# Optimization experiments

Measured on AMD Instinct MI355X. Metric: run time of the kernel, lower is better.

The kernel has to match this reference:

```python
import jax, jax.numpy as jnp
import numpy as np
from jax import lax

V, E, HD, T = 32000, 256, 256, 4   # vocab, embed dim, lstm hidden (bidir total), tagset (BMES)
H = HD // 2                        # hidden per direction
B, S = 64, 1024


def setup_inputs() -> dict:
    key = jax.random.key(0)
    ks = jax.random.split(key, 16)
    sc = 0.1
    return {
        "sentences": jax.random.randint(ks[0], (B, S), 0, V, dtype=jnp.int32),
        "embed": jax.random.normal(ks[1], (V, E), jnp.float32) * sc,
        "w_ih_f": jax.random.normal(ks[2], (4 * H, E), jnp.float32) * sc,
        "w_hh_f": jax.random.normal(ks[3], (4 * H, H), jnp.float32) * sc,
        "b_ih_f": jax.random.normal(ks[4], (4 * H,), jnp.float32) * sc,
        "b_hh_f": jax.random.normal(ks[5], (4 * H,), jnp.float32) * sc,
        "w_ih_r": jax.random.normal(ks[6], (4 * H, E), jnp.float32) * sc,
        "w_hh_r": jax.random.normal(ks[7], (4 * H, H), jnp.float32) * sc,
        "b_ih_r": jax.random.normal(ks[8], (4 * H,), jnp.float32) * sc,
        "b_hh_r": jax.random.normal(ks[9], (4 * H,), jnp.float32) * sc,
        "w_out": jax.random.normal(ks[10], (T, HD), jnp.float32) * sc,
        "b_out": jax.random.normal(ks[11], (T,), jnp.float32) * sc,
        "start_t": jax.random.normal(ks[12], (T,), jnp.float32) * sc,
        "end_t": jax.random.normal(ks[13], (T,), jnp.float32) * sc,
        "trans": jax.random.normal(ks[14], (T, T), jnp.float32) * sc,
    }


def _lstm_pass(x, w_ih, w_hh, b_ih, b_hh):
    # x: [S, B, E]; PyTorch gate order i, f, g, o; zero initial state.
    bsz = x.shape[1]
    hdim = w_hh.shape[1]
    b = b_ih + b_hh

    def step(carry, xt):
        h, c = carry
        z = xt @ w_ih.T + h @ w_hh.T + b  # [B, 4H]
        i, f, g, o = jnp.split(z, 4, axis=-1)
        c = jax.nn.sigmoid(f) * c + jax.nn.sigmoid(i) * jnp.tanh(g)
        h = jax.nn.sigmoid(o) * jnp.tanh(c)
        return (h, c), h

    init = (jnp.zeros((bsz, hdim), x.dtype), jnp.zeros((bsz, hdim), x.dtype))
    _, hs = lax.scan(step, init, x)
    return hs  # [S, B, H]


def _emissions(sentences, embed, w_ih_f, w_hh_f, b_ih_f, b_hh_f,
               w_ih_r, w_hh_r, b_ih_r, b_hh_r, w_out, b_out):
    x = embed[sentences]                # [B, S, E]
    xs = jnp.transpose(x, (1, 0, 2))    # [S, B, E]
    hf = _lstm_pass(xs, w_ih_f, w_hh_f, b_ih_f, b_hh_f)
    hr = _lstm_pass(xs[::-1], w_ih_r, w_hh_r, b_ih_r, b_hh_r)[::-1]
    h = jnp.concatenate([hf, hr], axis=-1)        # [S, B, 2H]
    return h @ w_out.T + b_out                    # [S, B, T] emissions


def _viterbi_decode(feats, start_t, end_t, trans):
    # feats: [S, B, T] (no mask: all sequences full length, matching crf.decode on dense batch)
    score0 = start_t + feats[0]  # [B, T]

    def fwd_step(score, emit):
        nxt = score[:, :, None] + trans[None, :, :] + emit[:, None, :]  # [B, Tprev, Tcur]
        return jnp.max(nxt, axis=1), jnp.argmax(nxt, axis=1)

    final, bps = lax.scan(fwd_step, score0, feats[1:])  # bps: [S-1, B, T]
    final = final + end_t
    last = jnp.argmax(final, axis=1)  # [B]

    def back_step(tag, bp):
        prev = jnp.take_along_axis(bp, tag[:, None], axis=1)[:, 0]
        return prev, prev

    _, path_head = lax.scan(back_step, last, bps, reverse=True)  # [S-1, B], tags at t=0..S-2
    path = jnp.concatenate([path_head, last[None]], axis=0)      # [S, B]
    return jnp.transpose(path, (1, 0)).astype(jnp.int32)         # [B, S]


def reference(sentences, embed, w_ih_f, w_hh_f, b_ih_f, b_hh_f,
              w_ih_r, w_hh_r, b_ih_r, b_hh_r, w_out, b_out,
              start_t, end_t, trans):
    feats = _emissions(sentences, embed, w_ih_f, w_hh_f, b_ih_f, b_hh_f,
                       w_ih_r, w_hh_r, b_ih_r, b_hh_r, w_out, b_out)
    return _viterbi_decode(feats, start_t, end_t, trans)
```

## Files before the change

### kernel.cpp

```cpp
#include <hip/hip_runtime.h>
#include <cstdint>
#include <cstddef>

#define SLEN 1024
#define BATCH 64
#define EDIM 256
#define HDIM 128
#define GDIM 512
#define NTAG 4

typedef float f2 __attribute__((ext_vector_type(2)));
typedef float f4 __attribute__((ext_vector_type(4)));


__device__ __forceinline__ float sigm_f(float x) {
    return 1.0f / (1.0f + __expf(-x));
}
__device__ __forceinline__ float tanh_f(float x) {
    return 1.0f - 2.0f / (1.0f + __expf(2.0f * x));
}

template <int CTRL>
__device__ __forceinline__ float quad_perm(float x) {
    return __int_as_float(
        __builtin_amdgcn_mov_dpp(__float_as_int(x), CTRL, 0xF, 0xF, true));
}
#define QP_XOR1 0xB1
#define QP_XOR2 0x4E
#define QP_MIR8 0x141
#define QP_BC0  0x00
#define QP_BC1  0x55
#define QP_BC2  0xAA
#define QP_BC3  0xFF

__device__ __forceinline__ void gemm_body(
    float* smem, int mt, int cp,
    const int* __restrict__ sent, const float* __restrict__ embed,
    const float* __restrict__ w_ih_f, const float* __restrict__ w_ih_r,
    const float* __restrict__ b_ih_f, const float* __restrict__ b_hh_f,
    const float* __restrict__ b_ih_r, const float* __restrict__ b_hh_r,
    float* __restrict__ Z, int base_f, int base_r)
{
    float* As = smem;
    const int t  = threadIdx.x;
    const int tm = t >> 8;
    const int tt = t & 255;
    float* Bs = smem + 4096 + tm * 4096;

    const int nt  = cp * 2 + tm;
    const int dir = nt >> 2;
    const float* W  = dir ? w_ih_r : w_ih_f;
    const float* bi = dir ? b_ih_r : b_ih_f;
    const float* bh = dir ? b_hh_r : b_hh_f;
    const int ncol = (nt & 3) * 128;
    const int r0   = mt * 128;

    const int sra = t & 127;
    const int qa  = t >> 7;
    const int r_loc = r0 + sra;
    const int s_loc = r_loc >> 6;
    const int b_    = r_loc & 63;
    const int s_glob = (dir ? base_r : base_f) + s_loc;
    const int tok = sent[b_ * SLEN + s_glob];
    const float* arow = embed + (size_t)tok * EDIM + qa * 8;

    const int srb = tt & 127;
    const int hb  = tt >> 7;
    const float* brow = W + (size_t)(ncol + srb) * EDIM + hb * 16;

    const int tx = tt & 15, ty = tt >> 4;

    f2 acc[8][4];
    #pragma unroll
    for (int i = 0; i < 8; ++i)
        #pragma unroll
        for (int jj = 0; jj < 4; ++jj) acc[i][jj] = (f2)(0.0f);

    for (int kt = 0; kt < 8; ++kt) {
        const int k0 = kt * 32;
        __syncthreads();
        {
            float4 v0 = *(const float4*)(arow + k0);
            float4 v1 = *(const float4*)(arow + k0 + 4);
            const int kk = qa * 8;
            As[(kk + 0) * 128 + sra] = v0.x;
            As[(kk + 1) * 128 + sra] = v0.y;
            As[(kk + 2) * 128 + sra] = v0.z;
            As[(kk + 3) * 128 + sra] = v0.w;
            As[(kk + 4) * 128 + sra] = v1.x;
            As[(kk + 5) * 128 + sra] = v1.y;
            As[(kk + 6) * 128 + sra] = v1.z;
            As[(kk + 7) * 128 + sra] = v1.w;
        }
        #pragma unroll
        for (int i = 0; i < 4; ++i) {
            float4 v = *(const float4*)(brow + k0 + i * 4);
            const int kk = hb * 16 + i * 4;
            Bs[(kk + 0) * 128 + srb] = v.x;
            Bs[(kk + 1) * 128 + srb] = v.y;
            Bs[(kk + 2) * 128 + srb] = v.z;
            Bs[(kk + 3) * 128 + srb] = v.w;
        }
        __syncthreads();

        #pragma unroll 8
        for (int k = 0; k < 32; ++k) {
            const f4 a0  = *(const f4*)&As[k * 128 + ty * 4];
            const f4 a1  = *(const f4*)&As[k * 128 + 64 + ty * 4];
            const f4 bq0 = *(const f4*)&Bs[k * 128 + tx * 4];
            const f4 bq1 = *(const f4*)&Bs[k * 128 + 64 + tx * 4];
            float av[8] = {a0.x, a0.y, a0.z, a0.w, a1.x, a1.y, a1.z, a1.w};
            f2 bv[4];
            bv[0] = __builtin_shufflevector(bq0, bq0, 0, 1);
            bv[1] = __builtin_shufflevector(bq0, bq0, 2, 3);
            bv[2] = __builtin_shufflevector(bq1, bq1, 0, 1);
            bv[3] = __builtin_shufflevector(bq1, bq1, 2, 3);
            #pragma unroll
            for (int i = 0; i < 8; ++i) {
                f2 as; as.x = av[i]; as.y = av[i];
                #pragma unroll
                for (int jj = 0; jj < 4; ++jj)
                    acc[i][jj] += as * bv[jj];
            }
        }
    }

    float bias0[4], bias1[4];
    #pragma unroll
    for (int j = 0; j < 4; ++j) {
        bias0[j] = bi[ncol + tx * 4 + j] + bh[ncol + tx * 4 + j];
        bias1[j] = bi[ncol + 64 + tx * 4 + j] + bh[ncol + 64 + tx * 4 + j];
    }

    #pragma unroll
    for (int i = 0; i < 8; ++i) {
        const int row = r0 + ((i < 4) ? (ty * 4 + i) : (64 + ty * 4 + i - 4));
        float* zp = Z + (size_t)row * 1024 + dir * 512 + ncol;
        float4 o0, o1;
        o0.x = acc[i][0].x + bias0[0]; o0.y = acc[i][0].y + bias0[1];
        o0.z = acc[i][1].x + bias0[2]; o0.w = acc[i][1].y + bias0[3];
        o1.x = acc[i][2].x + bias1[0]; o1.y = acc[i][2].y + bias1[1];
        o1.z = acc[i][3].x + bias1[2]; o1.w = acc[i][3].y + bias1[3];
        *(float4*)(zp + tx * 4)      = o0;
        *(float4*)(zp + 64 + tx * 4) = o1;
    }
}

__device__ __forceinline__ void lstm_body(
    float* smem,
    const float* __restrict__ Z, const float* __restrict__ w_hh_f,
    const float* __restrict__ w_hh_r, float* __restrict__ H,
    float* __restrict__ ST, int base_f, int base_r, int L, int first)
{
    float* sh_h = smem;

    const int bid = blockIdx.x;
    const int b   = bid & 63;
    const int dir = bid >> 6;
    const int q   = threadIdx.x;
    const int p   = q & 7;
    const int Q   = q >> 3;
    const int gt  = p & 3;
    const int hi  = p >> 2;
    const int u   = Q + hi * 64;

    const float* Whh = dir ? w_hh_r : w_hh_f;

    f2 w2[8][8];
    #pragma unroll
    for (int pr = 0; pr < 8; ++pr) {
        const int uu = (pr & 4) ? (Q + 64) : Q;
        const int gg = pr & 3;
        const f2* src =
            (const f2*)(Whh + ((size_t)(gg * 128 + uu) * 128 + p * 16));
        #pragma unroll
        for (int i = 0; i < 8; ++i) w2[pr][i] = src[i];
    }
    #pragma unroll
    for (int pr = 0; pr < 8; ++pr)
        #pragma unroll
        for (int i = 0; i < 8; ++i)
            asm volatile("" : "+v"(w2[pr][i]));

    float* stp = ST + (size_t)(dir * 64 + b) * 256;
    if (q < 128)
        sh_h[(q >> 5) * 36 + (q & 31)] = first ? 0.0f : stp[q];
    float c = first ? 0.0f : stp[128 + u];

    const ptrdiff_t zstride = dir ? -65536 : 65536;
    const float* zp0 = Z + (size_t)b * 1024 + dir * 512
                     + (dir ? (size_t)(L - 1) * 65536 : 0) + gt * 128 + u;
    const ptrdiff_t hstride = dir ? -16384 : 16384;
    float* hg = H + ((size_t)(dir ? (base_r + L - 1) : base_f) * 64 + b) * 256
              + dir * 128 + u;

    const bool k4 = (p & 4) != 0;
    const bool k2 = (p & 2) != 0;
    const bool k1 = (p & 1) != 0;
    const float gsc  = (gt == 2) ? 2.0f : 1.0f;
    const float gofs = (gt == 2) ? -1.0f : 0.0f;
    const int shr = (p >> 1) * 36 + (p & 1) * 16;
    const int shw = (u >> 5) * 36 + (u & 31);

    float zcur[4], znxt[4];
    {
        const float* zp = zp0;
        #pragma unroll
        for (int dt = 0; dt < 4; ++dt) { zcur[dt] = *zp; zp += zstride; }
    }
    __syncthreads();

    float hlast = 0.0f;

    for (int t0 = 0; t0 < L; t0 += 4) {
        const bool more = (t0 + 4 < L);
        if (more) {
            const float* zp = zp0 + (ptrdiff_t)(t0 + 4) * zstride;
            #pragma unroll
            for (int dt = 0; dt < 4; ++dt) { znxt[dt] = *zp; zp += zstride; }
        }

        #pragma unroll
        for (int dt = 0; dt < 4; ++dt) {
            const f4* hp = (const f4*)(sh_h + (dt & 1) * 160 + shr);
            f2 hv[8];
            #pragma unroll
            for (int i = 0; i < 4; ++i) {
                f4 v = hp[i];
                hv[2 * i]     = __builtin_shufflevector(v, v, 0, 1);
                hv[2 * i + 1] = __builtin_shufflevector(v, v, 2, 3);
            }
            float s[8];
            #pragma unroll
            for (int pr = 0; pr < 8; ++pr) {
                f2 a = (f2)(0.0f);
                #pragma unroll
                for (int i = 0; i < 8; ++i) a += w2[pr][i] * hv[i];
                s[pr] = a.x + a.y;
            }
            float K1[4];
            #pragma unroll
            for (int j = 0; j < 4; ++j) {
                float keep = k4 ? s[j + 4] : s[j];
                float send = k4 ? s[j] : s[j + 4];
                K1[j] = keep + quad_perm<QP_MIR8>(send);
            }
            float K2[2];
            #pragma unroll
            for (int j = 0; j < 2; ++j) {
                float keep = k2 ? K1[j + 2] : K1[j];
                float send = k2 ? K1[j] : K1[j + 2];
                K2[j] = keep + quad_perm<QP_XOR2>(send);
            }
            float keep3 = k1 ? K2[1] : K2[0];
            float send3 = k1 ? K2[0] : K2[1];
            float zv = keep3 + quad_perm<QP_XOR1>(send3) + zcur[dt];

            float sgv = sigm_f(zv * gsc);
            float act = fmaf(sgv, gsc, gofs);

            float a_i = quad_perm<QP_BC0>(act);
            float a_f = quad_perm<QP_BC1>(act);
            float a_g = quad_perm<QP_BC2>(act);
            float a_o = quad_perm<QP_BC3>(act);
            c = a_f * c + a_i * a_g;
            float h = a_o * tanh_f(c);
            hlast = h;

            if (gt == 0) {
                sh_h[((dt + 1) & 1) * 160 + shw] = h;
                *hg = h;
            }
            hg += hstride;
            __syncthreads();
        }

        if (more) {
            #pragma unroll
            for (int dt = 0; dt < 4; ++dt) zcur[dt] = znxt[dt];
        }
    }

    if (gt == 0) {
        stp[u] = hlast;
        stp[128 + u] = c;
    }
}

__global__ __launch_bounds__(512) void fused_lstm_gemm(
    const int* __restrict__ sent, const float* __restrict__ embed,
    const float* __restrict__ w_ih_f, const float* __restrict__ w_ih_r,
    const float* __restrict__ b_ih_f, const float* __restrict__ b_hh_f,
    const float* __restrict__ b_ih_r, const float* __restrict__ b_hh_r,
    float* __restrict__ Zw, int gbase_f, int gbase_r, int mtiles,
    const float* __restrict__ Zr, const float* __restrict__ w_hh_f,
    const float* __restrict__ w_hh_r, float* __restrict__ H,
    float* __restrict__ ST, int lbase_f, int lbase_r, int L, int first)
{
    __shared__ __align__(16) float smem[12288];

    if (blockIdx.x < 128) {
        lstm_body(smem, Zr, w_hh_f, w_hh_r, H, ST, lbase_f, lbase_r, L, first);
    } else {
        const int g  = blockIdx.x - 128;
        const int mt = g % mtiles;
        const int cp = g / mtiles;
        gemm_body(smem, mt, cp, sent, embed, w_ih_f, w_ih_r,
                  b_ih_f, b_hh_f, b_ih_r, b_hh_r, Zw, gbase_f, gbase_r);
    }
}

__global__ __launch_bounds__(512) void gemm_zin(
    const int* __restrict__ sent, const float* __restrict__ embed,
    const float* __restrict__ w_ih_f, const float* __restrict__ w_ih_r,
    const float* __restrict__ b_ih_f, const float* __restrict__ b_hh_f,
    const float* __restrict__ b_ih_r, const float* __restrict__ b_hh_r,
    float* __restrict__ Z, int base_f, int base_r)
{
    __shared__ __align__(16) float smem[12288];
    gemm_body(smem, blockIdx.x, blockIdx.y, sent, embed, w_ih_f, w_ih_r,
              b_ih_f, b_hh_f, b_ih_r, b_hh_r, Z, base_f, base_r);
}

__global__ __launch_bounds__(256) void emissions_k(
    const float* __restrict__ H, const float* __restrict__ w_out,
    const float* __restrict__ b_out, float* __restrict__ F)
{
    const int gid = blockIdx.x * 256 + threadIdx.x;
    const int r   = gid >> 2;
    const int tg  = gid & 3;
    const float4* h4 = (const float4*)(H + (size_t)r * 256);
    const float4* w4 = (const float4*)(w_out + (size_t)tg * 256);
    float a0 = 0.f, a1 = 0.f, a2 = 0.f, a3 = 0.f;
    #pragma unroll 8
    for (int k = 0; k < 64; ++k) {
        float4 h = h4[k], w = w4[k];
        a0 = fmaf(h.x, w.x, a0); a1 = fmaf(h.y, w.y, a1);
        a2 = fmaf(h.z, w.z, a2); a3 = fmaf(h.w, w.w, a3);
    }
    F[gid] = ((a0 + a1) + (a2 + a3)) + b_out[tg];
}

__device__ __forceinline__ unsigned compose_map(unsigned a, unsigned b) {
    unsigned r = 0;
    #pragma unroll
    for (int jj = 0; jj < 4; ++jj) {
        unsigned bj = (b >> (jj * 8)) & 3u;
        unsigned aj = (a >> (bj * 8)) & 3u;
        r |= aj << (jj * 8);
    }
    return r;
}

__global__ __launch_bounds__(64) void viterbi_k(
    const float* __restrict__ F, const float* __restrict__ start_t,
    const float* __restrict__ end_t, const float* __restrict__ trans,
    int* __restrict__ out)
{
    const int b    = blockIdx.x;
    const int lane = threadIdx.x;
    __shared__ __align__(16) float sfeat[SLEN][NTAG];
    __shared__ unsigned sbp[SLEN];

    #pragma unroll
    for (int i = 0; i < 16; ++i) {
        int s = i * 64 + lane;
        ((float4*)sfeat)[s] = *(const float4*)(F + ((size_t)s * BATCH + b) * NTAG);
    }
    __syncthreads();

    const int cur = lane & 3;
    float tr0 = trans[0 * 4 + cur], tr1 = trans[1 * 4 + cur];
    float tr2 = trans[2 * 4 + cur], tr3 = trans[3 * 4 + cur];
    float sc = start_t[cur] + sfeat[0][cur];

    for (int s = 1; s < SLEN; ++s) {
        float ft = sfeat[s][cur];
        float s0 = __shfl(sc, 0), s1 = __shfl(sc, 1);
        float s2 = __shfl(sc, 2), s3 = __shfl(sc, 3);
        float c0 = s0 + tr0, c1 = s1 + tr1, c2 = s2 + tr2, c3 = s3 + tr3;
        float best = c0; int arg = 0;
        if (c1 > best) { best = c1; arg = 1; }
        if (c2 > best) { best = c2; arg = 2; }
        if (c3 > best) { best = c3; arg = 3; }
        sc = best + ft;
        unsigned bp = (unsigned)arg;
        unsigned b0 = __shfl(bp, 0), b1 = __shfl(bp, 1);
        unsigned b2 = __shfl(bp, 2), b3 = __shfl(bp, 3);
        if (lane == 0) sbp[s] = b0 | (b1 << 8) | (b2 << 16) | (b3 << 24);
    }
    sc += end_t[cur];
    float f0 = __shfl(sc, 0), f1 = __shfl(sc, 1);
    float f2v = __shfl(sc, 2), f3 = __shfl(sc, 3);
    int last = 0; float bb = f0;
    if (f1 > bb)  { bb = f1;  last = 1; }
    if (f2v > bb) { bb = f2v; last = 2; }
    if (f3 > bb)  { bb = f3;  last = 3; }
    __syncthreads();

    unsigned m[16];
    #pragma unroll
    for (int k = 0; k < 16; ++k) {
        int s = lane * 16 + k;
        m[k] = (s >= 1) ? sbp[s] : 0x03020100u;
    }
    unsigned G = m[15];
    #pragma unroll
    for (int k = 14; k >= 0; --k) G = compose_map(m[k], G);
    unsigned R = G;
    #pragma unroll
    for (int d = 1; d < 64; d <<= 1) {
        unsigned oo = __shfl_down(R, d);
        if (lane + d < 64) R = compose_map(R, oo);
    }
    unsigned P = __shfl_down(R, 1);
    if (lane == 63) P = 0x03020100u;

    int tcur = (int)((P >> (last * 8)) & 3u);
    int* ob = out + b * SLEN + lane * 16;
    ob[15] = tcur;
    #pragma unroll
    for (int k = 15; k >= 1; --k) {
        tcur = (int)((m[k] >> (tcur * 8)) & 3u);
        ob[k - 1] = tcur;
    }
}

extern "C" void kernel_launch(void* const* d_in, const int* in_sizes, int n_in,
                              void* d_out, int out_size, void* d_ws, size_t ws_size,
                              hipStream_t stream)
{
    const int*   sent    = (const int*)d_in[0];
    const float* embed   = (const float*)d_in[1];
    const float* w_ih_f  = (const float*)d_in[2];
    const float* w_hh_f  = (const float*)d_in[3];
    const float* b_ih_f  = (const float*)d_in[4];
    const float* b_hh_f  = (const float*)d_in[5];
    const float* w_ih_r  = (const float*)d_in[6];
    const float* w_hh_r  = (const float*)d_in[7];
    const float* b_ih_r  = (const float*)d_in[8];
    const float* b_hh_r  = (const float*)d_in[9];
    const float* w_out   = (const float*)d_in[10];
    const float* b_out   = (const float*)d_in[11];
    const float* start_t = (const float*)d_in[12];
    const float* end_t   = (const float*)d_in[13];
    const float* trans   = (const float*)d_in[14];
    int* out = (int*)d_out;

    const size_t H_FLOATS  = (size_t)SLEN * BATCH * 256;
    const size_t F_FLOATS  = (size_t)SLEN * BATCH * NTAG;
    const size_t ST_FLOATS = (size_t)2 * BATCH * 256;
    const size_t FIXED = H_FLOATS + F_FLOATS + ST_FLOATS;

    int L = 0;
    for (int cand = 256; cand >= 32; cand >>= 1) {
        size_t need = ((size_t)2 * cand * BATCH * 1024 + FIXED) * sizeof(float);
        if (need <= ws_size) { L = cand; break; }
    }

    if (L > 0) {
        const int nch = SLEN / L;
        const int mtiles = (L * BATCH) / 128;
        float* Z0 = (float*)d_ws;
        float* Z1 = Z0 + (size_t)L * BATCH * 1024;
        float* H  = Z1 + (size_t)L * BATCH * 1024;
        float* F  = H + H_FLOATS;
        float* ST = F + F_FLOATS;
        float* Zb[2] = {Z0, Z1};

        gemm_zin<<<dim3(mtiles, 4), 512, 0, stream>>>(
            sent, embed, w_ih_f, w_ih_r, b_ih_f, b_hh_f, b_ih_r, b_hh_r,
            Zb[0], 0, SLEN - L);

        for (int c = 0; c < nch; ++c) {
            const int lbase_f = c * L;
            const int lbase_r = SLEN - (c + 1) * L;
            const int hasg = (c + 1 < nch);
            const int gbase_f = (c + 1) * L;
            const int gbase_r = SLEN - (c + 2) * L;
            const int grid = hasg ? (128 + mtiles * 4) : 128;
            fused_lstm_gemm<<<grid, 512, 0, stream>>>(
                sent, embed, w_ih_f, w_ih_r, b_ih_f, b_hh_f, b_ih_r, b_hh_r,
                Zb[(c + 1) & 1], hasg ? gbase_f : 0, hasg ? gbase_r : 0, mtiles,
                Zb[c & 1], w_hh_f, w_hh_r, H, ST, lbase_f, lbase_r, L,
                c == 0 ? 1 : 0);
        }

        emissions_k<<<1024, 256, 0, stream>>>(H, w_out, b_out, F);
        viterbi_k<<<64, 64, 0, stream>>>(F, start_t, end_t, trans, out);
    } else {
        int Ls = SLEN;
        while (Ls > 32) {
            size_t need = ((size_t)Ls * BATCH * 1024 + FIXED) * sizeof(float);
            if (need <= ws_size) break;
            Ls >>= 1;
        }
        const int nch = SLEN / Ls;
        const int mtiles = (Ls * BATCH) / 128;
        float* Z  = (float*)d_ws;
        float* H  = Z + (size_t)Ls * BATCH * 1024;
        float* F  = H + H_FLOATS;
        float* ST = F + F_FLOATS;

        for (int c = 0; c < nch; ++c) {
            const int base_f = c * Ls;
            const int base_r = SLEN - (c + 1) * Ls;
            gemm_zin<<<dim3(mtiles, 4), 512, 0, stream>>>(
                sent, embed, w_ih_f, w_ih_r, b_ih_f, b_hh_f, b_ih_r, b_hh_r,
                Z, base_f, base_r);
            fused_lstm_gemm<<<128, 512, 0, stream>>>(
                sent, embed, w_ih_f, w_ih_r, b_ih_f, b_hh_f, b_ih_r, b_hh_r,
                Z, 0, 0, mtiles,
                Z, w_hh_f, w_hh_r, H, ST, base_f, base_r, Ls, c == 0 ? 1 : 0);
        }
        emissions_k<<<1024, 256, 0, stream>>>(H, w_out, b_out, F);
        viterbi_k<<<64, 64, 0, stream>>>(F, start_t, end_t, trans, out);
    }
}
```

Measured before the change: 1.190 ms.

## Precompute per-vocab input-gate table and run the LSTM as one persistent kernel

Adds a path that computes embed·W_ihᵀ plus biases once per vocabulary entry into a 32000×1024 table. A single LSTM kernel then walks the whole sequence and gathers gate pre-activations by token id, prefetching four steps ahead. This replaces the per-chunk input GEMM over all B·S tokens and the chunked LSTM launches with their state save and restore. The GEMM shrinks from 65536 rows to 32000, at the cost of a large workspace table and scattered row reads during the recurrence. The old chunked path remains as a fallback when the workspace is too small.

```diff
diff --git a/kernel.cpp b/kernel.cpp
--- a/kernel.cpp
+++ b/kernel.cpp
@@ -8,6 +8,7 @@
 #define HDIM 128
 #define GDIM 512
 #define NTAG 4
+#define VOCAB 32000
 
 typedef float f2 __attribute__((ext_vector_type(2)));
 typedef float f4 __attribute__((ext_vector_type(4)));
@@ -33,20 +34,22 @@
 #define QP_BC2  0xAA
 #define QP_BC3  0xFF
 
-__device__ __forceinline__ void gemm_body(
-    float* smem, int mt, int cp,
-    const int* __restrict__ sent, const float* __restrict__ embed,
+__global__ __launch_bounds__(512) void table_k(
+    const float* __restrict__ embed,
     const float* __restrict__ w_ih_f, const float* __restrict__ w_ih_r,
     const float* __restrict__ b_ih_f, const float* __restrict__ b_hh_f,
     const float* __restrict__ b_ih_r, const float* __restrict__ b_hh_r,
-    float* __restrict__ Z, int base_f, int base_r)
-{
+    float* __restrict__ T)
+{
+    __shared__ __align__(16) float smem[12288];
     float* As = smem;
     const int t  = threadIdx.x;
     const int tm = t >> 8;
     const int tt = t & 255;
     float* Bs = smem + 4096 + tm * 4096;
 
+    const int mt  = blockIdx.x;
+    const int cp  = blockIdx.y;
     const int nt  = cp * 2 + tm;
     const int dir = nt >> 2;
     const float* W  = dir ? w_ih_r : w_ih_f;
@@ -57,12 +60,7 @@
 
     const int sra = t & 127;
     const int qa  = t >> 7;
-    const int r_loc = r0 + sra;
-    const int s_loc = r_loc >> 6;
-    const int b_    = r_loc & 63;
-    const int s_glob = (dir ? base_r : base_f) + s_loc;
-    const int tok = sent[b_ * SLEN + s_glob];
-    const float* arow = embed + (size_t)tok * EDIM + qa * 8;
+    const float* arow = embed + (size_t)(r0 + sra) * EDIM + qa * 8;
 
     const int srb = tt & 127;
     const int hb  = tt >> 7;
@@ -135,7 +133,7 @@
     #pragma unroll
     for (int i = 0; i < 8; ++i) {
         const int row = r0 + ((i < 4) ? (ty * 4 + i) : (64 + ty * 4 + i - 4));
-        float* zp = Z + (size_t)row * 1024 + dir * 512 + ncol;
+        float* zp = T + (size_t)row * 1024 + dir * 512 + ncol;
         float4 o0, o1;
         o0.x = acc[i][0].x + bias0[0]; o0.y = acc[i][0].y + bias0[1];
         o0.z = acc[i][1].x + bias0[2]; o0.w = acc[i][1].y + bias0[3];
@@ -146,13 +144,14 @@
     }
 }
 
-__device__ __forceinline__ void lstm_body(
-    float* smem,
-    const float* __restrict__ Z, const float* __restrict__ w_hh_f,
-    const float* __restrict__ w_hh_r, float* __restrict__ H,
-    float* __restrict__ ST, int base_f, int base_r, int L, int first)
-{
-    float* sh_h = smem;
+__global__ __launch_bounds__(512) __attribute__((amdgpu_waves_per_eu(2, 2)))
+void lstm_k(
+    const float* __restrict__ T, const int* __restrict__ sent,
+    const float* __restrict__ w_hh_f, const float* __restrict__ w_hh_r,
+    float* __restrict__ H)
+{
+    __shared__ __align__(16) float sh_h[320];
+    __shared__ int sh_tok[SLEN];
 
     const int bid = blockIdx.x;
     const int b   = bid & 63;
@@ -181,6 +180,248 @@
         #pragma unroll
         for (int i = 0; i < 8; ++i)
             asm volatile("" : "+v"(w2[pr][i]));
+
+    sh_tok[q]       = sent[b * SLEN + q];
+    sh_tok[512 + q] = sent[b * SLEN + 512 + q];
+    if (q < 128) sh_h[(q >> 5) * 36 + (q & 31)] = 0.0f;
+    float c = 0.0f;
+    __syncthreads();
+
+    const int zcol = dir * 512 + gt * 128 + u;
+    const ptrdiff_t hstride = dir ? -16384 : 16384;
+    float* hg = H + ((size_t)(dir ? (SLEN - 1) : 0) * 64 + b) * 256
+              + dir * 128 + u;
+
+    const bool k4 = (p & 4) != 0;
+    const bool k2 = (p & 2) != 0;
+    const bool k1 = (p & 1) != 0;
+    const float gsc  = (gt == 2) ? 2.0f : 1.0f;
+    const float gofs = (gt == 2) ? -1.0f : 0.0f;
+    const int shr = (p >> 1) * 36 + (p & 1) * 16;
+    const int shw = (u >> 5) * 36 + (u & 31);
+
+    float zcur[4], znxt[4];
+    #pragma unroll
+    for (int dt = 0; dt < 4; ++dt) {
+        const int s = dir ? (SLEN - 1 - dt) : dt;
+        zcur[dt] = T[((size_t)sh_tok[s] << 10) + zcol];
+    }
+
+    for (int t0 = 0; t0 < SLEN; t0 += 4) {
+        const bool more = (t0 + 4 < SLEN);
+        if (more) {
+            #pragma unroll
+            for (int dt = 0; dt < 4; ++dt) {
+                const int tn = t0 + 4 + dt;
+                const int s = dir ? (SLEN - 1 - tn) : tn;
+                znxt[dt] = T[((size_t)sh_tok[s] << 10) + zcol];
+            }
+        }
+
+        #pragma unroll
+        for (int dt = 0; dt < 4; ++dt) {
+            const f4* hp = (const f4*)(sh_h + (dt & 1) * 160 + shr);
+            f2 hv[8];
+            #pragma unroll
+            for (int i = 0; i < 4; ++i) {
+                f4 v = hp[i];
+                hv[2 * i]     = __builtin_shufflevector(v, v, 0, 1);
+                hv[2 * i + 1] = __builtin_shufflevector(v, v, 2, 3);
+            }
+            float s[8];
+            #pragma unroll
+            for (int pr = 0; pr < 8; ++pr) {
+                f2 a = (f2)(0.0f);
+                #pragma unroll
+                for (int i = 0; i < 8; ++i) a += w2[pr][i] * hv[i];
+                s[pr] = a.x + a.y;
+            }
+            float K1[4];
+            #pragma unroll
+            for (int j = 0; j < 4; ++j) {
+                float keep = k4 ? s[j + 4] : s[j];
+                float send = k4 ? s[j] : s[j + 4];
+                K1[j] = keep + quad_perm<QP_MIR8>(send);
+            }
+            float K2[2];
+            #pragma unroll
+            for (int j = 0; j < 2; ++j) {
+                float keep = k2 ? K1[j + 2] : K1[j];
+                float send = k2 ? K1[j] : K1[j + 2];
+                K2[j] = keep + quad_perm<QP_XOR2>(send);
+            }
+            float keep3 = k1 ? K2[1] : K2[0];
+            float send3 = k1 ? K2[0] : K2[1];
+            float zv = keep3 + quad_perm<QP_XOR1>(send3) + zcur[dt];
+
+            float sgv = sigm_f(zv * gsc);
+            float act = fmaf(sgv, gsc, gofs);
+
+            float a_i = quad_perm<QP_BC0>(act);
+            float a_f = quad_perm<QP_BC1>(act);
+            float a_g = quad_perm<QP_BC2>(act);
+            float a_o = quad_perm<QP_BC3>(act);
+            c = a_f * c + a_i * a_g;
+            float h = a_o * tanh_f(c);
+
+            if (gt == 0) {
+                sh_h[((dt + 1) & 1) * 160 + shw] = h;
+                *hg = h;
+            }
+            hg += hstride;
+            __syncthreads();
+        }
+
+        if (more) {
+            #pragma unroll
+            for (int dt = 0; dt < 4; ++dt) zcur[dt] = znxt[dt];
+        }
+    }
+}
+
+__device__ __forceinline__ void gemm_body(
+    float* smem, int mt, int cp,
+    const int* __restrict__ sent, const float* __restrict__ embed,
+    const float* __restrict__ w_ih_f, const float* __restrict__ w_ih_r,
+    const float* __restrict__ b_ih_f, const float* __restrict__ b_hh_f,
+    const float* __restrict__ b_ih_r, const float* __restrict__ b_hh_r,
+    float* __restrict__ Z, int base_f, int base_r)
+{
+    float* As = smem;
+    const int t  = threadIdx.x;
+    const int tm = t >> 8;
+    const int tt = t & 255;
+    float* Bs = smem + 4096 + tm * 4096;
+
+    const int nt  = cp * 2 + tm;
+    const int dir = nt >> 2;
+    const float* W  = dir ? w_ih_r : w_ih_f;
+    const float* bi = dir ? b_ih_r : b_ih_f;
+    const float* bh = dir ? b_hh_r : b_hh_f;
+    const int ncol = (nt & 3) * 128;
+    const int r0   = mt * 128;
+
+    const int sra = t & 127;
+    const int qa  = t >> 7;
+    const int r_loc = r0 + sra;
+    const int s_loc = r_loc >> 6;
+    const int b_    = r_loc & 63;
+    const int s_glob = (dir ? base_r : base_f) + s_loc;
+    const int tok = sent[b_ * SLEN + s_glob];
+    const float* arow = embed + (size_t)tok * EDIM + qa * 8;
+
+    const int srb = tt & 127;
+    const int hb  = tt >> 7;
+    const float* brow = W + (size_t)(ncol + srb) * EDIM + hb * 16;
+
+    const int tx = tt & 15, ty = tt >> 4;
+
+    f2 acc[8][4];
+    #pragma unroll
+    for (int i = 0; i < 8; ++i)
+        #pragma unroll
+        for (int jj = 0; jj < 4; ++jj) acc[i][jj] = (f2)(0.0f);
+
+    for (int kt = 0; kt < 8; ++kt) {
+        const int k0 = kt * 32;
+        __syncthreads();
+        {
+            float4 v0 = *(const float4*)(arow + k0);
+            float4 v1 = *(const float4*)(arow + k0 + 4);
+            const int kk = qa * 8;
+            As[(kk + 0) * 128 + sra] = v0.x;
+            As[(kk + 1) * 128 + sra] = v0.y;
+            As[(kk + 2) * 128 + sra] = v0.z;
+            As[(kk + 3) * 128 + sra] = v0.w;
+            As[(kk + 4) * 128 + sra] = v1.x;
+            As[(kk + 5) * 128 + sra] = v1.y;
+            As[(kk + 6) * 128 + sra] = v1.z;
+            As[(kk + 7) * 128 + sra] = v1.w;
+        }
+        #pragma unroll
+        for (int i = 0; i < 4; ++i) {
+            float4 v = *(const float4*)(brow + k0 + i * 4);
+            const int kk = hb * 16 + i * 4;
+            Bs[(kk + 0) * 128 + srb] = v.x;
+            Bs[(kk + 1) * 128 + srb] = v.y;
+            Bs[(kk + 2) * 128 + srb] = v.z;
+            Bs[(kk + 3) * 128 + srb] = v.w;
+        }
+        __syncthreads();
+
+        #pragma unroll 8
+        for (int k = 0; k < 32; ++k) {
+            const f4 a0  = *(const f4*)&As[k * 128 + ty * 4];
+            const f4 a1  = *(const f4*)&As[k * 128 + 64 + ty * 4];
+            const f4 bq0 = *(const f4*)&Bs[k * 128 + tx * 4];
+            const f4 bq1 = *(const f4*)&Bs[k * 128 + 64 + tx * 4];
+            float av[8] = {a0.x, a0.y, a0.z, a0.w, a1.x, a1.y, a1.z, a1.w};
+            f2 bv[4];
+            bv[0] = __builtin_shufflevector(bq0, bq0, 0, 1);
+            bv[1] = __builtin_shufflevector(bq0, bq0, 2, 3);
+            bv[2] = __builtin_shufflevector(bq1, bq1, 0, 1);
+            bv[3] = __builtin_shufflevector(bq1, bq1, 2, 3);
+            #pragma unroll
+            for (int i = 0; i < 8; ++i) {
+                f2 as; as.x = av[i]; as.y = av[i];
+                #pragma unroll
+                for (int jj = 0; jj < 4; ++jj)
+                    acc[i][jj] += as * bv[jj];
+            }
+        }
+    }
+
+    float bias0[4], bias1[4];
+    #pragma unroll
+    for (int j = 0; j < 4; ++j) {
+        bias0[j] = bi[ncol + tx * 4 + j] + bh[ncol + tx * 4 + j];
+        bias1[j] = bi[ncol + 64 + tx * 4 + j] + bh[ncol + 64 + tx * 4 + j];
+    }
+
+    #pragma unroll
+    for (int i = 0; i < 8; ++i) {
+        const int row = r0 + ((i < 4) ? (ty * 4 + i) : (64 + ty * 4 + i - 4));
+        float* zp = Z + (size_t)row * 1024 + dir * 512 + ncol;
+        float4 o0, o1;
+        o0.x = acc[i][0].x + bias0[0]; o0.y = acc[i][0].y + bias0[1];
+        o0.z = acc[i][1].x + bias0[2]; o0.w = acc[i][1].y + bias0[3];
+        o1.x = acc[i][2].x + bias1[0]; o1.y = acc[i][2].y + bias1[1];
+        o1.z = acc[i][3].x + bias1[2]; o1.w = acc[i][3].y + bias1[3];
+        *(float4*)(zp + tx * 4)      = o0;
+        *(float4*)(zp + 64 + tx * 4) = o1;
+    }
+}
+
+__device__ __forceinline__ void lstm_body(
+    float* smem,
+    const float* __restrict__ Z, const float* __restrict__ w_hh_f,
+    const float* __restrict__ w_hh_r, float* __restrict__ H,
+    float* __restrict__ ST, int base_f, int base_r, int L, int first)
+{
+    float* sh_h = smem;
+
+    const int bid = blockIdx.x;
+    const int b   = bid & 63;
+    const int dir = bid >> 6;
+    const int q   = threadIdx.x;
+    const int p   = q & 7;
+    const int Q   = q >> 3;
+    const int gt  = p & 3;
+    const int hi  = p >> 2;
+    const int u   = Q + hi * 64;
+
+    const float* Whh = dir ? w_hh_r : w_hh_f;
+
+    f2 w2[8][8];
+    #pragma unroll
+    for (int pr = 0; pr < 8; ++pr) {
+        const int uu = (pr & 4) ? (Q + 64) : Q;
+        const int gg = pr & 3;
+        const f2* src =
+            (const f2*)(Whh + ((size_t)(gg * 128 + uu) * 128 + p * 16));
+        #pragma unroll
+        for (int i = 0; i < 8; ++i) w2[pr][i] = src[i];
+    }
 
     float* stp = ST + (size_t)(dir * 64 + b) * 256;
     if (q < 128)
@@ -449,9 +690,25 @@
 
     const size_t H_FLOATS  = (size_t)SLEN * BATCH * 256;
     const size_t F_FLOATS  = (size_t)SLEN * BATCH * NTAG;
+    const size_t T_FLOATS  = (size_t)VOCAB * 1024;
     const size_t ST_FLOATS = (size_t)2 * BATCH * 256;
+
+    const size_t table_need = (T_FLOATS + H_FLOATS + F_FLOATS) * sizeof(float);
+
+    if (ws_size >= table_need) {
+        float* T = (float*)d_ws;
+        float* H = T + T_FLOATS;
+        float* F = H + H_FLOATS;
+
+        table_k<<<dim3(250, 4), 512, 0, stream>>>(
+            embed, w_ih_f, w_ih_r, b_ih_f, b_hh_f, b_ih_r, b_hh_r, T);
+        lstm_k<<<128, 512, 0, stream>>>(T, sent, w_hh_f, w_hh_r, H);
+        emissions_k<<<1024, 256, 0, stream>>>(H, w_out, b_out, F);
+        viterbi_k<<<64, 64, 0, stream>>>(F, start_t, end_t, trans, out);
+        return;
+    }
+
     const size_t FIXED = H_FLOATS + F_FLOATS + ST_FLOATS;
-
     int L = 0;
     for (int cand = 256; cand >= 32; cand >>= 1) {
         size_t need = ((size_t)2 * cand * BATCH * 1024 + FIXED) * sizeof(float);
```

After: 1.122 ms (median of 3 runs). 5.7% less time.
